# Performance work log

Measured on AMD Instinct MI355X. Metric: run time of the kernel, lower is better.

The kernel has to match this reference:

```python
import jax, jax.numpy as jnp
import numpy as np

# FocalLossAdaptive (Mukhoti et al. FLSD): per-sample gamma from pt thresholds
# gamma_dic = {0.2: 5.0, 0.5: 3.0}; pt >= 0.5 -> self.gamma (=3.0)
GAMMA_SELF = 3.0
GAMMA_LT_02 = 5.0
GAMMA_LT_05 = 3.0

N, C = 4096, 32000

def setup_inputs() -> dict:
    key = jax.random.key(0)
    k1, k2 = jax.random.split(key)
    input = jax.random.normal(k1, (N, C), dtype=jnp.float32)
    target = jax.random.randint(k2, (N,), 0, C, dtype=jnp.int64)
    return {"input": input, "target": target}

def reference(input, target):
    # logpt[i] = log_softmax(input)[i, target[i]]
    logpt = jnp.take_along_axis(
        jax.nn.log_softmax(input, axis=1), target[:, None], axis=1
    )[:, 0]
    pt = jnp.exp(logpt)
    # vectorized replacement of the per-sample Python loop:
    gamma = jnp.where(pt >= 0.5, GAMMA_SELF,
                      jnp.where(pt < 0.2, GAMMA_LT_02, GAMMA_LT_05))
    loss = -((1.0 - pt) ** gamma) * logpt
    return jnp.sum(loss)  # size_average=False -> sum
```

## Files before the change

kernel.cpp:

```cpp
#include <hip/hip_runtime.h>
#include <float.h>


#define BLOCK 256
#define NSTR 4

__device__ __forceinline__ void merge_chunk(float& m, float& s, float c, float e) {
  float M = fmaxf(m, c);
  float d = __expf(fminf(m, c) - M);
  s = (c > m) ? fmaf(s, d, e) : fmaf(e, d, s);
  m = M;
}

__global__ __launch_bounds__(BLOCK) void focal_row_kernel(
    const float* __restrict__ input,
    const int* __restrict__ target,
    float* __restrict__ row_loss,
    int C) {
  const int row = blockIdx.x;
  const int tid = threadIdx.x;
  const float* __restrict__ rowp = input + (size_t)row * (size_t)C;
  const float4* __restrict__ row4 = reinterpret_cast<const float4*>(rowp);

  float m[NSTR], s[NSTR];
#pragma unroll
  for (int j = 0; j < NSTR; ++j) { m[j] = -FLT_MAX; s[j] = 0.0f; }

  const int nvec = C >> 2;
  int k = tid;
  for (; k + (NSTR - 1) * BLOCK < nvec; k += NSTR * BLOCK) {
    float4 v[NSTR];
#pragma unroll
    for (int j = 0; j < NSTR; ++j) v[j] = row4[k + j * BLOCK];
#pragma unroll
    for (int j = 0; j < NSTR; ++j) {
      float c = fmaxf(fmaxf(v[j].x, v[j].y), fmaxf(v[j].z, v[j].w));
      float e = __expf(v[j].x - c) + __expf(v[j].y - c) +
                __expf(v[j].z - c) + __expf(v[j].w - c);
      merge_chunk(m[j], s[j], c, e);
    }
  }
  for (; k < nvec; k += BLOCK) {
    float4 v = row4[k];
    float c = fmaxf(fmaxf(v.x, v.y), fmaxf(v.z, v.w));
    float e = __expf(v.x - c) + __expf(v.y - c) +
              __expf(v.z - c) + __expf(v.w - c);
    merge_chunk(m[0], s[0], c, e);
  }
  for (int i = (nvec << 2) + tid; i < C; i += BLOCK) {
    merge_chunk(m[0], s[0], rowp[i], 1.0f);
  }

#pragma unroll
  for (int j = 1; j < NSTR; ++j) {
    float M = fmaxf(m[0], m[j]);
    float d = __expf(fminf(m[0], m[j]) - M);
    s[0] = (m[j] > m[0]) ? fmaf(s[0], d, s[j]) : fmaf(s[j], d, s[0]);
    m[0] = M;
  }
  float mm = m[0], ss = s[0];

#pragma unroll
  for (int off = 32; off > 0; off >>= 1) {
    float mo = __shfl_down(mm, off);
    float so = __shfl_down(ss, off);
    float M = fmaxf(mm, mo);
    ss = ss * __expf(mm - M) + so * __expf(mo - M);
    mm = M;
  }

  __shared__ float sm[BLOCK / 64];
  __shared__ float sw[BLOCK / 64];
  const int wave = tid >> 6;
  const int lane = tid & 63;
  if (lane == 0) { sm[wave] = mm; sw[wave] = ss; }
  __syncthreads();

  if (tid == 0) {
    const int nw = BLOCK / 64;
    float M = sm[0];
#pragma unroll
    for (int w = 1; w < nw; ++w) M = fmaxf(M, sm[w]);
    float S = 0.0f;
#pragma unroll
    for (int w = 0; w < nw; ++w) S += sw[w] * __expf(sm[w] - M);

    const int t = target[row];
    const float xt = rowp[t];
    const float logpt = xt - M - __logf(S);
    const float pt = __expf(logpt);
    const float om = 1.0f - pt;
    const float w3 = om * om * om;
    const float wgt = (pt < 0.2f) ? w3 * om * om : w3;
    row_loss[row] = -wgt * logpt;
  }
}

__global__ __launch_bounds__(BLOCK) void reduce_kernel(
    const float* __restrict__ row_loss, float* __restrict__ out, int N) {
  const int tid = threadIdx.x;
  float s = 0.0f;
  for (int i = tid; i < N; i += BLOCK) s += row_loss[i];
#pragma unroll
  for (int off = 32; off > 0; off >>= 1) s += __shfl_down(s, off);
  __shared__ float sw[BLOCK / 64];
  if ((tid & 63) == 0) sw[tid >> 6] = s;
  __syncthreads();
  if (tid == 0) out[0] = sw[0] + sw[1] + sw[2] + sw[3];
}

extern "C" void kernel_launch(void* const* d_in, const int* in_sizes, int n_in,
                              void* d_out, int out_size, void* d_ws, size_t ws_size,
                              hipStream_t stream) {
  const float* input = (const float*)d_in[0];
  const int* target = (const int*)d_in[1];
  float* out = (float*)d_out;
  float* row_loss = (float*)d_ws;

  const int N = in_sizes[1];
  const int C = in_sizes[0] / N;

  focal_row_kernel<<<dim3(N), dim3(BLOCK), 0, stream>>>(input, target, row_loss, C);
  reduce_kernel<<<dim3(1), dim3(BLOCK), 0, stream>>>(row_loss, out, N);
}
```

Baseline: 661.8 us.

## Split each row across four blocks with partial softmax merged in finalize kernel

Each row is now handled by SPLIT=4 blocks, each computing a partial (max, sum) online softmax over its segment of the 32000 columns. The block whose segment holds the target writes the target logit. A single 1024-thread finalize kernel merges the partials per row, computes the focal loss and sums it. The aim is more blocks and shorter per-block loops to raise memory-level parallelism. The cost is extra workspace traffic and slightly more merge work.

New measurement: 661.0 us. About the same (-0.1%).

```diff
diff --git a/kernel.cpp b/kernel.cpp
--- a/kernel.cpp
+++ b/kernel.cpp
@@ -4,6 +4,8 @@
 
 #define BLOCK 256
 #define NSTR 4
+#define SPLIT 4
+#define BLK2 1024
 
 __device__ __forceinline__ void merge_chunk(float& m, float& s, float c, float e) {
   float M = fmaxf(m, c);
@@ -12,23 +14,38 @@
   m = M;
 }
 
-__global__ __launch_bounds__(BLOCK) void focal_row_kernel(
+__global__ __launch_bounds__(BLOCK) void partial_softmax_kernel(
     const float* __restrict__ input,
     const int* __restrict__ target,
-    float* __restrict__ row_loss,
+    float2* __restrict__ partial,
+    float* __restrict__ xt_out,
     int C) {
-  const int row = blockIdx.x;
+  const int bid = blockIdx.x;
+  const int row = bid / SPLIT;
+  const int seg = bid % SPLIT;
+  const int N = gridDim.x / SPLIT;
   const int tid = threadIdx.x;
   const float* __restrict__ rowp = input + (size_t)row * (size_t)C;
   const float4* __restrict__ row4 = reinterpret_cast<const float4*>(rowp);
+
+  const int nvec = C >> 2;
+  const int segLen = nvec / SPLIT;
+  const int base = seg * segLen;
+  const int end = (seg == SPLIT - 1) ? nvec : base + segLen;
+
+  if (tid == 0) {
+    const int t = target[row];
+    const int fbeg = base << 2;
+    const int fend = (seg == SPLIT - 1) ? C : (end << 2);
+    if (t >= fbeg && t < fend) xt_out[row] = rowp[t];
+  }
 
   float m[NSTR], s[NSTR];
 #pragma unroll
   for (int j = 0; j < NSTR; ++j) { m[j] = -FLT_MAX; s[j] = 0.0f; }
 
-  const int nvec = C >> 2;
-  int k = tid;
-  for (; k + (NSTR - 1) * BLOCK < nvec; k += NSTR * BLOCK) {
+  int k = base + tid;
+  for (; k + (NSTR - 1) * BLOCK < end; k += NSTR * BLOCK) {
     float4 v[NSTR];
 #pragma unroll
     for (int j = 0; j < NSTR; ++j) v[j] = row4[k + j * BLOCK];
@@ -40,15 +57,17 @@
       merge_chunk(m[j], s[j], c, e);
     }
   }
-  for (; k < nvec; k += BLOCK) {
+  for (; k < end; k += BLOCK) {
     float4 v = row4[k];
     float c = fmaxf(fmaxf(v.x, v.y), fmaxf(v.z, v.w));
     float e = __expf(v.x - c) + __expf(v.y - c) +
               __expf(v.z - c) + __expf(v.w - c);
     merge_chunk(m[0], s[0], c, e);
   }
-  for (int i = (nvec << 2) + tid; i < C; i += BLOCK) {
-    merge_chunk(m[0], s[0], rowp[i], 1.0f);
+  if (seg == SPLIT - 1) {
+    for (int i = (nvec << 2) + tid; i < C; i += BLOCK) {
+      merge_chunk(m[0], s[0], rowp[i], 1.0f);
+    }
   }
 
 #pragma unroll
@@ -84,29 +103,47 @@
     float S = 0.0f;
 #pragma unroll
     for (int w = 0; w < nw; ++w) S += sw[w] * __expf(sm[w] - M);
+    partial[seg * N + row] = make_float2(M, S);
+  }
+}
 
-    const int t = target[row];
-    const float xt = rowp[t];
-    const float logpt = xt - M - __logf(S);
-    const float pt = __expf(logpt);
+__global__ __launch_bounds__(BLK2) void finalize_kernel(
+    const float2* __restrict__ partial,
+    const float* __restrict__ xt,
+    float* __restrict__ out, int N) {
+  const int tid = threadIdx.x;
+  float lsum = 0.0f;
+
+  for (int r = tid; r < N; r += BLK2) {
+    float2 p[SPLIT];
+#pragma unroll
+    for (int g = 0; g < SPLIT; ++g) p[g] = partial[g * N + r];
+    float M = p[0].x;
+#pragma unroll
+    for (int g = 1; g < SPLIT; ++g) M = fmaxf(M, p[g].x);
+    float S = 0.0f;
+#pragma unroll
+    for (int g = 0; g < SPLIT; ++g) S += p[g].y * expf(p[g].x - M);
+
+    const float logpt = xt[r] - M - logf(S);
+    const float pt = expf(logpt);
     const float om = 1.0f - pt;
     const float w3 = om * om * om;
     const float wgt = (pt < 0.2f) ? w3 * om * om : w3;
-    row_loss[row] = -wgt * logpt;
+    lsum += -wgt * logpt;
   }
-}
 
-__global__ __launch_bounds__(BLOCK) void reduce_kernel(
-    const float* __restrict__ row_loss, float* __restrict__ out, int N) {
-  const int tid = threadIdx.x;
-  float s = 0.0f;
-  for (int i = tid; i < N; i += BLOCK) s += row_loss[i];
 #pragma unroll
-  for (int off = 32; off > 0; off >>= 1) s += __shfl_down(s, off);
-  __shared__ float sw[BLOCK / 64];
-  if ((tid & 63) == 0) sw[tid >> 6] = s;
+  for (int off = 32; off > 0; off >>= 1) lsum += __shfl_down(lsum, off);
+  __shared__ float sw[BLK2 / 64];
+  if ((tid & 63) == 0) sw[tid >> 6] = lsum;
   __syncthreads();
-  if (tid == 0) out[0] = sw[0] + sw[1] + sw[2] + sw[3];
+  if (tid == 0) {
+    float s = 0.0f;
+#pragma unroll
+    for (int w = 0; w < BLK2 / 64; ++w) s += sw[w];
+    out[0] = s;
+  }
 }
 
 extern "C" void kernel_launch(void* const* d_in, const int* in_sizes, int n_in,
@@ -115,11 +152,14 @@
   const float* input = (const float*)d_in[0];
   const int* target = (const int*)d_in[1];
   float* out = (float*)d_out;
-  float* row_loss = (float*)d_ws;
 
   const int N = in_sizes[1];
   const int C = in_sizes[0] / N;
 
-  focal_row_kernel<<<dim3(N), dim3(BLOCK), 0, stream>>>(input, target, row_loss, C);
-  reduce_kernel<<<dim3(1), dim3(BLOCK), 0, stream>>>(row_loss, out, N);
+  float2* partial = (float2*)d_ws;
+  float* xt = (float*)((char*)d_ws + (size_t)SPLIT * N * sizeof(float2));
+
+  partial_softmax_kernel<<<dim3(N * SPLIT), dim3(BLOCK), 0, stream>>>(
+      input, target, partial, xt, C);
+  finalize_kernel<<<dim3(1), dim3(BLK2), 0, stream>>>(partial, xt, out, N);
 }
```
